# Kernel optimization log

Hardware: AMD Instinct MI355X
Metric: run time of the kernel (lower is better)

## Reference

```python
import jax, jax.numpy as jnp
import numpy as np

C = 64; H = 80; W = 160; B = 3; L = 4
REC = [4, 3, 2]  # agents per scene, sum = 9
EPS = 1e-5
NEG = -1e30  # stands in for -inf (numerically identical after softmax)


def setup_inputs() -> dict:
    key = jax.random.key(0)
    ks = jax.random.split(key, 24)
    def p(i, shape, s=0.05):
        return s * jax.random.normal(ks[i], shape, jnp.float32)
    x = jax.random.normal(ks[0], (sum(REC), C, H, W), jnp.float32)
    mask = jnp.ones((B, L, H, W), jnp.float32)
    record_len = jnp.array(REC, jnp.int32)
    eye = jnp.broadcast_to(jnp.array([[1., 0., 0.], [0., 1., 0.]], jnp.float32), (B, L, L, 2, 3))
    noise = 0.05 * jax.random.normal(ks[1], (B, L, L, 2, 3), jnp.float32)
    diag = jnp.eye(L, dtype=bool)[None, :, :, None, None]
    pairwise_t_matrix = jnp.where(diag, eye, eye + noise)  # near-identity normalized affines
    inp = dict(x=x, mask=mask, record_len=record_len, pairwise_t_matrix=pairwise_t_matrix)
    chans = [(2 * C, 128), (128, 32), (32, 8)]
    for n, (ci, co) in zip([1, 2, 3], chans):
        inp[f'w{n}'] = p(2 * n, (ci, co))
        inp[f'cb{n}'] = p(2 * n + 1, (co,), 0.01)
        inp[f'g{n}'] = 1.0 + p(8 + n, (co,), 0.1)
        inp[f'be{n}'] = p(12 + n, (co,), 0.1)
        inp[f'rm{n}'] = jnp.zeros((co,), jnp.float32)
        inp[f'rv{n}'] = jnp.ones((co,), jnp.float32)
    inp['w4'] = p(16, (8, 1)); inp['cb4'] = p(17, (1,), 0.01)
    inp['mlp_w'] = p(18, (C, C)); inp['mlp_b'] = p(19, (C,), 0.01)
    return inp


def _bilinear(feat, px, py):
    # feat [C,H,W]; px,py [H,W] source pixel coords; zero padding outside
    x0 = jnp.floor(px); y0 = jnp.floor(py)
    wx = px - x0; wy = py - y0
    x0i = x0.astype(jnp.int32); y0i = y0.astype(jnp.int32)
    def gat(xi, yi):
        inb = ((xi >= 0) & (xi < W) & (yi >= 0) & (yi < H)).astype(feat.dtype)
        v = feat[:, jnp.clip(yi, 0, H - 1), jnp.clip(xi, 0, W - 1)]
        return v * inb
    return (gat(x0i, y0i) * (1 - wx) * (1 - wy) + gat(x0i + 1, y0i) * wx * (1 - wy)
            + gat(x0i, y0i + 1) * (1 - wx) * wy + gat(x0i + 1, y0i + 1) * wx * wy)


def _warp_one(feat, theta):
    # torch affine_grid convention: src_norm = theta @ [x_n, y_n, 1]
    ys = jnp.linspace(-1.0, 1.0, H); xs = jnp.linspace(-1.0, 1.0, W)
    gx, gy = jnp.meshgrid(xs, ys)  # [H,W]
    sx = theta[0, 0] * gx + theta[0, 1] * gy + theta[0, 2]
    sy = theta[1, 0] * gx + theta[1, 1] * gy + theta[1, 2]
    px = (sx + 1.0) * (W - 1) / 2.0
    py = (sy + 1.0) * (H - 1) / 2.0
    return _bilinear(feat, px, py)

_warp_j = jax.vmap(_warp_one, in_axes=(0, 0))        # over neighbor j
_warp_ij = jax.vmap(_warp_j, in_axes=(None, 0))      # over ego i
_warp_bij = jax.vmap(_warp_ij, in_axes=(0, 0))       # over scene b


def _forward(x, mask, rec, ptm, w1, cb1, g1, be1, rm1, rv1, w2, cb2, g2, be2, rm2, rv2,
             w3, cb3, g3, be3, rm3, rv3, w4, cb4, mlp_w, mlp_b):
    # regroup: pad per-scene agent features to [B,L,C,H,W]
    feats, idx = [], 0
    for n in rec:
        feats.append(jnp.pad(x[idx:idx + n], ((0, L - n), (0, 0), (0, 0), (0, 0))))
        idx += n
    node = jnp.stack(feats)                                      # [B,L,C,H,W]
    valid = jnp.asarray((np.asarray(rec)[:, None] > np.arange(L)).astype(np.float32))  # [B,L]
    theta = jnp.swapaxes(ptm, 1, 2)                              # theta[b,i,j] = ptm[b,j,i]
    nbr = _warp_bij(node, theta)                                 # [B,L,L,C,H,W]
    wm = _warp_bij(mask[:, :, None], theta)                      # [B,L,L,1,H,W] warped ROI masks
    com_mask = wm * valid[:, None, :, None, None, None]
    ego = jnp.broadcast_to(node[:, :, None], nbr.shape)          # ego feature repeated over j
    z = jnp.concatenate([nbr, ego], axis=3)                      # [B,L,L,2C,H,W]

    def conv_bn_relu(t, w, cb, g, be, rm, rv):
        t = jnp.einsum('bijchw,co->bijohw', t, w) + cb[:, None, None]
        t = (t - rm[:, None, None]) * (g[:, None, None] / jnp.sqrt(rv[:, None, None] + EPS)) + be[:, None, None]
        return jax.nn.relu(t)

    h = conv_bn_relu(z, w1, cb1, g1, be1, rm1, rv1)
    h = conv_bn_relu(h, w2, cb2, g2, be2, rm2, rv2)
    h = conv_bn_relu(h, w3, cb3, g3, be3, rm3, rv3)
    s = jax.nn.relu(jnp.einsum('bijchw,co->bijohw', h, w4) + cb4[:, None, None])  # [B,L,L,1,H,W]
    s = jnp.where(com_mask == 0, NEG, s)
    aw = jax.nn.softmax(s, axis=2)                               # softmax over neighbors j
    updated = jnp.sum(aw * nbr * com_mask, axis=2)               # [B,L,C,H,W]
    out = updated[:, 0]                                          # ego agent per scene [B,C,H,W]
    return jnp.einsum('bchw,cd->bdhw', out, mlp_w) + mlp_b[:, None, None]


def reference(x, mask, record_len, pairwise_t_matrix, w1, cb1, g1, be1, rm1, rv1,
              w2, cb2, g2, be2, rm2, rv2, w3, cb3, g3, be3, rm3, rv3, w4, cb4, mlp_w, mlp_b):
    rec = [int(v) for v in np.asarray(record_len)]
    return _forward(x, mask, rec, pairwise_t_matrix, w1, cb1, g1, be1, rm1, rv1,
                    w2, cb2, g2, be2, rm2, rv2, w3, cb3, g3, be3, rm3, rv3, w4, cb4, mlp_w, mlp_b)
```

## Files before the change

### kernel.cpp

```cpp
#include <hip/hip_runtime.h>
#include <math.h>

#define CC 64
#define HH 80
#define WW 160
#define BB 3
#define LL 4
#define HW (HH * WW)
#define EPSf 1e-5f
#define NEGf -1e30f

typedef __attribute__((ext_vector_type(8))) short bf16x8;
typedef __attribute__((ext_vector_type(4))) float f32x4;

union BU { unsigned short s[8]; bf16x8 v; };

__device__ __forceinline__ unsigned short f2bf(float f) {
    unsigned int u = __float_as_uint(f);
    u = u + 0x7fffu + ((u >> 16) & 1u);
    return (unsigned short)(u >> 16);
}
__device__ __forceinline__ float b2f(unsigned short h) {
    return __uint_as_float(((unsigned int)h) << 16);
}

__device__ __forceinline__ void src_xy(const float* __restrict__ th, int pix,
                                       float& px, float& py) {
    int w = pix % WW, h = pix / WW;
    float gx = -1.f + 2.f * (float)w / (float)(WW - 1);
    float gy = -1.f + 2.f * (float)h / (float)(HH - 1);
    float sx = th[0] * gx + th[1] * gy + th[2];
    float sy = th[3] * gx + th[4] * gy + th[5];
    px = (sx + 1.f) * (float)(WW - 1) * 0.5f;
    py = (sy + 1.f) * (float)(HH - 1) * 0.5f;
}

struct Tap { int a00, a01, a10, a11; float w00, w01, w10, w11; };

__device__ __forceinline__ Tap mk_tap(float px, float py) {
    Tap tp;
    float x0f = floorf(px), y0f = floorf(py);
    float wx = px - x0f, wy = py - y0f;
    int x0 = (int)x0f, y0 = (int)y0f, x1 = x0 + 1, y1 = y0 + 1;
    float bx0 = (x0 >= 0 && x0 < WW) ? 1.f : 0.f;
    float bx1 = (x1 >= 0 && x1 < WW) ? 1.f : 0.f;
    float by0 = (y0 >= 0 && y0 < HH) ? 1.f : 0.f;
    float by1 = (y1 >= 0 && y1 < HH) ? 1.f : 0.f;
    int xc0 = min(max(x0, 0), WW - 1), xc1 = min(max(x1, 0), WW - 1);
    int yc0 = min(max(y0, 0), HH - 1), yc1 = min(max(y1, 0), HH - 1);
    tp.w00 = (1.f - wx) * (1.f - wy) * bx0 * by0;
    tp.w01 = wx * (1.f - wy) * bx1 * by0;
    tp.w10 = (1.f - wx) * wy * bx0 * by1;
    tp.w11 = wx * wy * bx1 * by1;
    tp.a00 = yc0 * WW + xc0; tp.a01 = yc0 * WW + xc1;
    tp.a10 = yc1 * WW + xc0; tp.a11 = yc1 * WW + xc1;
    return tp;
}


__global__ __launch_bounds__(256) void k_prep(
    const float* __restrict__ w1, const float* __restrict__ w2,
    const float* __restrict__ mlpw,
    const float* __restrict__ cb1, const float* __restrict__ g1,
    const float* __restrict__ be1, const float* __restrict__ rm1, const float* __restrict__ rv1,
    const float* __restrict__ cb2, const float* __restrict__ g2,
    const float* __restrict__ be2, const float* __restrict__ rm2, const float* __restrict__ rv2,
    const float* __restrict__ cb3, const float* __restrict__ g3,
    const float* __restrict__ be3, const float* __restrict__ rm3, const float* __restrict__ rv3,
    unsigned short* __restrict__ w1T, unsigned short* __restrict__ w2T,
    unsigned short* __restrict__ mwT,
    float* __restrict__ kk1, float* __restrict__ bb1,
    float* __restrict__ kk2, float* __restrict__ bb2,
    float* __restrict__ kk3, float* __restrict__ bb3)
{
    int idx = blockIdx.x * 256 + threadIdx.x;
    if (idx < 16384) {
        int o = idx >> 7, c = idx & 127;
        w1T[idx] = f2bf(w1[c * 128 + o]);
    } else if (idx < 20480) {
        int i = idx - 16384;
        int o2 = i >> 7, o = i & 127;
        w2T[i] = f2bf(w2[o * 32 + o2]);
    } else if (idx < 24576) {
        int i = idx - 20480;
        int d = i >> 6, c = i & 63;
        mwT[i] = f2bf(mlpw[c * 64 + d]);
    } else if (idx < 24704) {
        int o = idx - 24576;
        float k = g1[o] * rsqrtf(rv1[o] + EPSf);
        kk1[o] = k; bb1[o] = fmaf(cb1[o] - rm1[o], k, be1[o]);
    } else if (idx < 24736) {
        int o = idx - 24704;
        float k = g2[o] * rsqrtf(rv2[o] + EPSf);
        kk2[o] = k; bb2[o] = fmaf(cb2[o] - rm2[o], k, be2[o]);
    } else if (idx < 24744) {
        int o = idx - 24736;
        float k = g3[o] * rsqrtf(rv3[o] + EPSf);
        kk3[o] = k; bb3[o] = fmaf(cb3[o] - rm3[o], k, be3[o]);
    }
}


__global__ __launch_bounds__(256, 2) void k_fused(
    const float* __restrict__ x, const float* __restrict__ mask,
    const int* __restrict__ rec, const float* __restrict__ ptm,
    const unsigned short* __restrict__ w1T, const unsigned short* __restrict__ w2T,
    const unsigned short* __restrict__ mwT,
    const float* __restrict__ kk1, const float* __restrict__ bb1,
    const float* __restrict__ kk2, const float* __restrict__ bb2,
    const float* __restrict__ kk3, const float* __restrict__ bb3,
    const float* __restrict__ w3, const float* __restrict__ w4,
    const float* __restrict__ cb4, const float* __restrict__ mlp_b,
    float* __restrict__ out)
{
    __shared__ unsigned short H1s[64 * 136];
    __shared__ float H2f[64 * 36];
    __shared__ float s_s[4 * 64];
    __shared__ float com_s[4 * 64];

    int t = threadIdx.x;
    int b = blockIdx.x / 200, tile = blockIdx.x % 200;
    int pix0 = tile * 64;
    int wave = t >> 6, lane = t & 63, q = lane >> 4, r16 = lane & 15;
    int p = wave * 16 + r16;
    int pix = pix0 + p;

    int r0 = rec[0], r1 = rec[1], r2 = rec[2];
    int rb = (b == 0) ? r0 : ((b == 1) ? r1 : r2);
    int off = (b >= 1 ? r0 : 0) + (b >= 2 ? r1 : 0);

    float kv1[8], bv1[8];
    #pragma unroll
    for (int nt = 0; nt < 8; ++nt) { int o = nt * 16 + r16; kv1[nt] = kk1[o]; bv1[nt] = bb1[o]; }
    float kv2[2], bv2[2];
    #pragma unroll
    for (int nt = 0; nt < 2; ++nt) { int o = nt * 16 + r16; kv2[nt] = kk2[o]; bv2[nt] = bb2[o]; }

    bf16x8 e0, e1;
    {
        BU u0, u1;
        const float* xe = x + (size_t)off * CC * HW + pix;
        #pragma unroll
        for (int i = 0; i < 8; ++i) {
            u0.s[i] = f2bf(xe[(size_t)(q * 8 + i) * HW]);
            u1.s[i] = f2bf(xe[(size_t)(32 + q * 8 + i) * HW]);
        }
        e0 = u0.v; e1 = u1.v;
    }

    const f32x4 z4 = {0.f, 0.f, 0.f, 0.f};
    bf16x8 nbrA[8];

    #pragma unroll
    for (int j = 0; j < 4; ++j) {
        bf16x8 a0 = {0,0,0,0,0,0,0,0}, a1 = {0,0,0,0,0,0,0,0};
        bool valid = j < rb;
        if (valid) {
            const float* th = ptm + ((size_t)(b * 4 + j) * 4) * 6;
            float px, py; src_xy(th, pix, px, py);
            Tap tp = mk_tap(px, py);
            const float* feat = x + (size_t)(off + j) * CC * HW;
            BU u0, u1;
            #pragma unroll
            for (int i = 0; i < 8; ++i) {
                const float* f0 = feat + (size_t)(q * 8 + i) * HW;
                float v0 = tp.w00 * f0[tp.a00] + tp.w01 * f0[tp.a01]
                         + tp.w10 * f0[tp.a10] + tp.w11 * f0[tp.a11];
                u0.s[i] = f2bf(v0);
                const float* f1 = feat + (size_t)(32 + q * 8 + i) * HW;
                float v1 = tp.w00 * f1[tp.a00] + tp.w01 * f1[tp.a01]
                         + tp.w10 * f1[tp.a10] + tp.w11 * f1[tp.a11];
                u1.s[i] = f2bf(v1);
            }
            a0 = u0.v; a1 = u1.v;

            f32x4 acc1[8];
            #pragma unroll
            for (int nt = 0; nt < 8; ++nt) acc1[nt] = z4;
            #pragma unroll
            for (int ks = 0; ks < 4; ++ks) {
                bf16x8 A = (ks == 0) ? a0 : (ks == 1) ? a1 : (ks == 2) ? e0 : e1;
                int kcol = ks * 32 + q * 8;
                #pragma unroll
                for (int nt = 0; nt < 8; ++nt) {
                    bf16x8 bf = *(const bf16x8*)(w1T + (size_t)(nt * 16 + r16) * 128 + kcol);
                    acc1[nt] = __builtin_amdgcn_mfma_f32_16x16x32_bf16(A, bf, acc1[nt], 0, 0, 0);
                }
            }
            #pragma unroll
            for (int nt = 0; nt < 8; ++nt) {
                #pragma unroll
                for (int r = 0; r < 4; ++r) {
                    float h = fmaxf(fmaf(acc1[nt][r], kv1[nt], bv1[nt]), 0.f);
                    H1s[(wave * 16 + q * 4 + r) * 136 + nt * 16 + r16] = f2bf(h);
                }
            }
            f32x4 acc2[2]; acc2[0] = z4; acc2[1] = z4;
            #pragma unroll
            for (int ks = 0; ks < 4; ++ks) {
                int kcol = ks * 32 + q * 8;
                bf16x8 A = *(const bf16x8*)&H1s[(wave * 16 + r16) * 136 + kcol];
                #pragma unroll
                for (int nt = 0; nt < 2; ++nt) {
                    bf16x8 bf = *(const bf16x8*)(w2T + (size_t)(nt * 16 + r16) * 128 + kcol);
                    acc2[nt] = __builtin_amdgcn_mfma_f32_16x16x32_bf16(A, bf, acc2[nt], 0, 0, 0);
                }
            }
            #pragma unroll
            for (int nt = 0; nt < 2; ++nt) {
                #pragma unroll
                for (int r = 0; r < 4; ++r) {
                    float h = fmaxf(fmaf(acc2[nt][r], kv2[nt], bv2[nt]), 0.f);
                    H2f[(wave * 16 + q * 4 + r) * 36 + nt * 16 + r16] = h;
                }
            }
        }
        __syncthreads();
        if (t < 64) {
            if (valid) {
                const float* th = ptm + ((size_t)(b * 4 + j) * 4) * 6;
                float px, py; src_xy(th, pix0 + t, px, py);
                Tap tp = mk_tap(px, py);
                const float* mk = mask + (size_t)(b * 4 + j) * HW;
                float wm = tp.w00 * mk[tp.a00] + tp.w01 * mk[tp.a01]
                         + tp.w10 * mk[tp.a10] + tp.w11 * mk[tp.a11];
                float a3[8];
                #pragma unroll
                for (int o = 0; o < 8; ++o) a3[o] = 0.f;
                #pragma unroll 4
                for (int c = 0; c < 32; ++c) {
                    float hv = H2f[t * 36 + c];
                    #pragma unroll
                    for (int o = 0; o < 8; ++o) a3[o] = fmaf(hv, w3[c * 8 + o], a3[o]);
                }
                float s = cb4[0];
                #pragma unroll
                for (int o = 0; o < 8; ++o) {
                    float h = fmaxf(fmaf(a3[o], kk3[o], bb3[o]), 0.f);
                    s = fmaf(h, w4[o], s);
                }
                s = fmaxf(s, 0.f);
                s_s[j * 64 + t] = (wm == 0.f) ? NEGf : s;
                com_s[j * 64 + t] = wm;
            } else {
                s_s[j * 64 + t] = NEGf;
                com_s[j * 64 + t] = 0.f;
            }
        }
        __syncthreads();
        nbrA[j * 2 + 0] = a0;
        nbrA[j * 2 + 1] = a1;
    }

    float sj[4], cj[4];
    #pragma unroll
    for (int j = 0; j < 4; ++j) { sj[j] = s_s[j * 64 + p]; cj[j] = com_s[j * 64 + p]; }
    float m = fmaxf(fmaxf(sj[0], sj[1]), fmaxf(sj[2], sj[3]));
    float e[4], sum = 0.f;
    #pragma unroll
    for (int j = 0; j < 4; ++j) { e[j] = __expf(sj[j] - m); sum += e[j]; }
    float inv = 1.f / sum;
    float wgt[4];
    #pragma unroll
    for (int j = 0; j < 4; ++j) wgt[j] = e[j] * inv * cj[j];

    float u0f[8], u1f[8];
    #pragma unroll
    for (int i = 0; i < 8; ++i) { u0f[i] = 0.f; u1f[i] = 0.f; }
    #pragma unroll
    for (int j = 0; j < 4; ++j) {
        float wj = wgt[j];
        #pragma unroll
        for (int i = 0; i < 8; ++i) {
            u0f[i] = fmaf(wj, b2f((unsigned short)nbrA[j * 2 + 0][i]), u0f[i]);
            u1f[i] = fmaf(wj, b2f((unsigned short)nbrA[j * 2 + 1][i]), u1f[i]);
        }
    }
    BU p0, p1;
    #pragma unroll
    for (int i = 0; i < 8; ++i) { p0.s[i] = f2bf(u0f[i]); p1.s[i] = f2bf(u1f[i]); }

    f32x4 acc3[4];
    #pragma unroll
    for (int nt = 0; nt < 4; ++nt) acc3[nt] = z4;
    #pragma unroll
    for (int ks = 0; ks < 2; ++ks) {
        bf16x8 A = ks ? p1.v : p0.v;
        int kcol = ks * 32 + q * 8;
        #pragma unroll
        for (int nt = 0; nt < 4; ++nt) {
            bf16x8 bf = *(const bf16x8*)(mwT + (size_t)(nt * 16 + r16) * 64 + kcol);
            acc3[nt] = __builtin_amdgcn_mfma_f32_16x16x32_bf16(A, bf, acc3[nt], 0, 0, 0);
        }
    }

    float* outT = (float*)H1s;
    #pragma unroll
    for (int nt = 0; nt < 4; ++nt) {
        int d = nt * 16 + r16;
        float mb = mlp_b[d];
        #pragma unroll
        for (int r = 0; r < 4; ++r)
            outT[d * 65 + wave * 16 + q * 4 + r] = acc3[nt][r] + mb;
    }
    __syncthreads();
    {
        int p2 = t & 63, dg = t >> 6;
        #pragma unroll
        for (int i = 0; i < 16; ++i) {
            int d = dg * 16 + i;
            out[((size_t)(b * CC + d)) * HW + pix0 + p2] = outT[d * 65 + p2];
        }
    }
}


extern "C" void kernel_launch(void* const* d_in, const int* in_sizes, int n_in,
                              void* d_out, int out_size, void* d_ws, size_t ws_size,
                              hipStream_t stream)
{
    const float* x    = (const float*)d_in[0];
    const float* mask = (const float*)d_in[1];
    const int*   rec  = (const int*)  d_in[2];
    const float* ptm  = (const float*)d_in[3];
    const float* w1   = (const float*)d_in[4];
    const float* cb1  = (const float*)d_in[5];
    const float* g1   = (const float*)d_in[6];
    const float* be1  = (const float*)d_in[7];
    const float* rm1  = (const float*)d_in[8];
    const float* rv1  = (const float*)d_in[9];
    const float* w2   = (const float*)d_in[10];
    const float* cb2  = (const float*)d_in[11];
    const float* g2   = (const float*)d_in[12];
    const float* be2  = (const float*)d_in[13];
    const float* rm2  = (const float*)d_in[14];
    const float* rv2  = (const float*)d_in[15];
    const float* w3   = (const float*)d_in[16];
    const float* cb3  = (const float*)d_in[17];
    const float* g3   = (const float*)d_in[18];
    const float* be3  = (const float*)d_in[19];
    const float* rm3  = (const float*)d_in[20];
    const float* rv3  = (const float*)d_in[21];
    const float* w4   = (const float*)d_in[22];
    const float* cb4  = (const float*)d_in[23];
    const float* mlpw = (const float*)d_in[24];
    const float* mlpb = (const float*)d_in[25];
    float* out = (float*)d_out;

    unsigned short* w1T = (unsigned short*)d_ws;
    unsigned short* w2T = w1T + 16384;
    unsigned short* mwT = w2T + 4096;
    float* kk1 = (float*)(mwT + 4096);
    float* bb1 = kk1 + 128;
    float* kk2 = bb1 + 128;
    float* bb2 = kk2 + 32;
    float* kk3 = bb2 + 32;
    float* bb3 = kk3 + 8;

    k_prep<<<dim3(97), dim3(256), 0, stream>>>(
        w1, w2, mlpw, cb1, g1, be1, rm1, rv1, cb2, g2, be2, rm2, rv2,
        cb3, g3, be3, rm3, rv3, w1T, w2T, mwT, kk1, bb1, kk2, bb2, kk3, bb3);

    k_fused<<<dim3(600), dim3(256), 0, stream>>>(
        x, mask, rec, ptm, w1T, w2T, mwT,
        kk1, bb1, kk2, bb2, kk3, bb3,
        w3, w4, cb4, mlpb, out);
}
```

Before: 177.1 us.

## Map neighbor agents to waves with 16-pixel tiles instead of looping per block

Each block now covers 16 pixels instead of 64, and each of its four waves handles one neighbor agent in parallel. This replaces the serial loop over neighbors and its two barriers per iteration with a single barrier. Warped neighbor features go through shared memory rather than registers, and the mask-weighted score head runs in each wave's first quarter-wave. The grid grows fourfold, launch bounds target higher occupancy, and output stores become float4. The cost is that waves for absent agents sit idle, the ego features are reloaded by every wave, and the small tiles give shorter coalesced runs on gathers and stores.

Result: slower. 181.7 us (+2.6%).

```diff
diff --git a/kernel.cpp b/kernel.cpp
--- a/kernel.cpp
+++ b/kernel.cpp
@@ -101,7 +101,7 @@
 }
 
 
-__global__ __launch_bounds__(256, 2) void k_fused(
+__global__ __launch_bounds__(256, 5) void k_fused(
     const float* __restrict__ x, const float* __restrict__ mask,
     const int* __restrict__ rec, const float* __restrict__ ptm,
     const unsigned short* __restrict__ w1T, const unsigned short* __restrict__ w2T,
@@ -113,148 +113,138 @@
     const float* __restrict__ cb4, const float* __restrict__ mlp_b,
     float* __restrict__ out)
 {
-    __shared__ unsigned short H1s[64 * 136];
-    __shared__ float H2f[64 * 36];
-    __shared__ float s_s[4 * 64];
-    __shared__ float com_s[4 * 64];
+    __shared__ __align__(16) char pool[27136];
+    unsigned short* nbr_s = (unsigned short*)pool;
+    unsigned short* H1s   = (unsigned short*)(pool + 9216);
+    float* s_s   = (float*)(pool + 26624);
+    float* com_s = (float*)(pool + 26880);
 
     int t = threadIdx.x;
-    int b = blockIdx.x / 200, tile = blockIdx.x % 200;
-    int pix0 = tile * 64;
+    int b = blockIdx.x / 800, tile = blockIdx.x % 800;
+    int pix0 = tile * 16;
     int wave = t >> 6, lane = t & 63, q = lane >> 4, r16 = lane & 15;
-    int p = wave * 16 + r16;
-    int pix = pix0 + p;
+    int pix = pix0 + r16;
 
     int r0 = rec[0], r1 = rec[1], r2 = rec[2];
     int rb = (b == 0) ? r0 : ((b == 1) ? r1 : r2);
     int off = (b >= 1 ? r0 : 0) + (b >= 2 ? r1 : 0);
-
-    float kv1[8], bv1[8];
-    #pragma unroll
-    for (int nt = 0; nt < 8; ++nt) { int o = nt * 16 + r16; kv1[nt] = kk1[o]; bv1[nt] = bb1[o]; }
-    float kv2[2], bv2[2];
-    #pragma unroll
-    for (int nt = 0; nt < 2; ++nt) { int o = nt * 16 + r16; kv2[nt] = kk2[o]; bv2[nt] = bb2[o]; }
-
-    bf16x8 e0, e1;
-    {
+    bool valid = (wave < rb);
+
+    unsigned short* Hw = H1s + wave * (16 * 136);
+    float* H2w = (float*)Hw;
+    const f32x4 z4 = {0.f, 0.f, 0.f, 0.f};
+
+    if (valid) {
+        const float* th = ptm + (size_t)(b * 4 + wave) * 24;
+        float px_, py_; src_xy(th, pix, px_, py_);
+        Tap tp = mk_tap(px_, py_);
+        const float* feat = x + (size_t)(off + wave) * CC * HW;
         BU u0, u1;
+        #pragma unroll
+        for (int i = 0; i < 8; ++i) {
+            const float* f0 = feat + (size_t)(q * 8 + i) * HW;
+            float v0 = tp.w00 * f0[tp.a00] + tp.w01 * f0[tp.a01]
+                     + tp.w10 * f0[tp.a10] + tp.w11 * f0[tp.a11];
+            u0.s[i] = f2bf(v0);
+            const float* f1 = feat + (size_t)(32 + q * 8 + i) * HW;
+            float v1 = tp.w00 * f1[tp.a00] + tp.w01 * f1[tp.a01]
+                     + tp.w10 * f1[tp.a10] + tp.w11 * f1[tp.a11];
+            u1.s[i] = f2bf(v1);
+        }
+        float wm = 0.f;
+        if (q == 0) {
+            const float* mk = mask + (size_t)(b * 4 + wave) * HW;
+            wm = tp.w00 * mk[tp.a00] + tp.w01 * mk[tp.a01]
+               + tp.w10 * mk[tp.a10] + tp.w11 * mk[tp.a11];
+        }
+        *(bf16x8*)&nbr_s[(wave * 16 + r16) * 72 + q * 8]      = u0.v;
+        *(bf16x8*)&nbr_s[(wave * 16 + r16) * 72 + 32 + q * 8] = u1.v;
+
+        BU v0u, v1u;
         const float* xe = x + (size_t)off * CC * HW + pix;
         #pragma unroll
         for (int i = 0; i < 8; ++i) {
-            u0.s[i] = f2bf(xe[(size_t)(q * 8 + i) * HW]);
-            u1.s[i] = f2bf(xe[(size_t)(32 + q * 8 + i) * HW]);
-        }
-        e0 = u0.v; e1 = u1.v;
-    }
-
-    const f32x4 z4 = {0.f, 0.f, 0.f, 0.f};
-    bf16x8 nbrA[8];
-
-    #pragma unroll
-    for (int j = 0; j < 4; ++j) {
-        bf16x8 a0 = {0,0,0,0,0,0,0,0}, a1 = {0,0,0,0,0,0,0,0};
-        bool valid = j < rb;
-        if (valid) {
-            const float* th = ptm + ((size_t)(b * 4 + j) * 4) * 6;
-            float px, py; src_xy(th, pix, px, py);
-            Tap tp = mk_tap(px, py);
-            const float* feat = x + (size_t)(off + j) * CC * HW;
-            BU u0, u1;
-            #pragma unroll
-            for (int i = 0; i < 8; ++i) {
-                const float* f0 = feat + (size_t)(q * 8 + i) * HW;
-                float v0 = tp.w00 * f0[tp.a00] + tp.w01 * f0[tp.a01]
-                         + tp.w10 * f0[tp.a10] + tp.w11 * f0[tp.a11];
-                u0.s[i] = f2bf(v0);
-                const float* f1 = feat + (size_t)(32 + q * 8 + i) * HW;
-                float v1 = tp.w00 * f1[tp.a00] + tp.w01 * f1[tp.a01]
-                         + tp.w10 * f1[tp.a10] + tp.w11 * f1[tp.a11];
-                u1.s[i] = f2bf(v1);
-            }
-            a0 = u0.v; a1 = u1.v;
-
-            f32x4 acc1[8];
-            #pragma unroll
-            for (int nt = 0; nt < 8; ++nt) acc1[nt] = z4;
-            #pragma unroll
-            for (int ks = 0; ks < 4; ++ks) {
-                bf16x8 A = (ks == 0) ? a0 : (ks == 1) ? a1 : (ks == 2) ? e0 : e1;
-                int kcol = ks * 32 + q * 8;
+            v0u.s[i] = f2bf(xe[(size_t)(q * 8 + i) * HW]);
+            v1u.s[i] = f2bf(xe[(size_t)(32 + q * 8 + i) * HW]);
+        }
+
+        f32x4 acc1[8];
+        #pragma unroll
+        for (int nt = 0; nt < 8; ++nt) acc1[nt] = z4;
+        #pragma unroll
+        for (int ks = 0; ks < 4; ++ks) {
+            bf16x8 A = (ks == 0) ? u0.v : (ks == 1) ? u1.v : (ks == 2) ? v0u.v : v1u.v;
+            int kcol = ks * 32 + q * 8;
+            #pragma unroll
+            for (int nt = 0; nt < 8; ++nt) {
+                bf16x8 bw = *(const bf16x8*)(w1T + (size_t)(nt * 16 + r16) * 128 + kcol);
+                acc1[nt] = __builtin_amdgcn_mfma_f32_16x16x32_bf16(A, bw, acc1[nt], 0, 0, 0);
+            }
+        }
+        #pragma unroll
+        for (int nt = 0; nt < 8; ++nt) {
+            int o = nt * 16 + r16;
+            float kv = kk1[o], bv = bb1[o];
+            #pragma unroll
+            for (int r = 0; r < 4; ++r) {
+                float h = fmaxf(fmaf(acc1[nt][r], kv, bv), 0.f);
+                Hw[(q * 4 + r) * 136 + o] = f2bf(h);
+            }
+        }
+
+        f32x4 acc2[2]; acc2[0] = z4; acc2[1] = z4;
+        #pragma unroll
+        for (int ks = 0; ks < 4; ++ks) {
+            int kcol = ks * 32 + q * 8;
+            bf16x8 A = *(const bf16x8*)&Hw[r16 * 136 + kcol];
+            #pragma unroll
+            for (int nt = 0; nt < 2; ++nt) {
+                bf16x8 bw = *(const bf16x8*)(w2T + (size_t)(nt * 16 + r16) * 128 + kcol);
+                acc2[nt] = __builtin_amdgcn_mfma_f32_16x16x32_bf16(A, bw, acc2[nt], 0, 0, 0);
+            }
+        }
+        #pragma unroll
+        for (int nt = 0; nt < 2; ++nt) {
+            int o = nt * 16 + r16;
+            float kv = kk2[o], bv = bb2[o];
+            #pragma unroll
+            for (int r = 0; r < 4; ++r) {
+                float h = fmaxf(fmaf(acc2[nt][r], kv, bv), 0.f);
+                H2w[(q * 4 + r) * 36 + o] = h;
+            }
+        }
+
+        if (q == 0) {
+            float a3[8];
+            #pragma unroll
+            for (int o = 0; o < 8; ++o) a3[o] = 0.f;
+            #pragma unroll 4
+            for (int c = 0; c < 32; ++c) {
+                float hv = H2w[r16 * 36 + c];
                 #pragma unroll
-                for (int nt = 0; nt < 8; ++nt) {
-                    bf16x8 bf = *(const bf16x8*)(w1T + (size_t)(nt * 16 + r16) * 128 + kcol);
-                    acc1[nt] = __builtin_amdgcn_mfma_f32_16x16x32_bf16(A, bf, acc1[nt], 0, 0, 0);
-                }
-            }
-            #pragma unroll
-            for (int nt = 0; nt < 8; ++nt) {
-                #pragma unroll
-                for (int r = 0; r < 4; ++r) {
-                    float h = fmaxf(fmaf(acc1[nt][r], kv1[nt], bv1[nt]), 0.f);
-                    H1s[(wave * 16 + q * 4 + r) * 136 + nt * 16 + r16] = f2bf(h);
-                }
-            }
-            f32x4 acc2[2]; acc2[0] = z4; acc2[1] = z4;
-            #pragma unroll
-            for (int ks = 0; ks < 4; ++ks) {
-                int kcol = ks * 32 + q * 8;
-                bf16x8 A = *(const bf16x8*)&H1s[(wave * 16 + r16) * 136 + kcol];
-                #pragma unroll
-                for (int nt = 0; nt < 2; ++nt) {
-                    bf16x8 bf = *(const bf16x8*)(w2T + (size_t)(nt * 16 + r16) * 128 + kcol);
-                    acc2[nt] = __builtin_amdgcn_mfma_f32_16x16x32_bf16(A, bf, acc2[nt], 0, 0, 0);
-                }
-            }
-            #pragma unroll
-            for (int nt = 0; nt < 2; ++nt) {
-                #pragma unroll
-                for (int r = 0; r < 4; ++r) {
-                    float h = fmaxf(fmaf(acc2[nt][r], kv2[nt], bv2[nt]), 0.f);
-                    H2f[(wave * 16 + q * 4 + r) * 36 + nt * 16 + r16] = h;
-                }
-            }
-        }
-        __syncthreads();
-        if (t < 64) {
-            if (valid) {
-                const float* th = ptm + ((size_t)(b * 4 + j) * 4) * 6;
-                float px, py; src_xy(th, pix0 + t, px, py);
-                Tap tp = mk_tap(px, py);
-                const float* mk = mask + (size_t)(b * 4 + j) * HW;
-                float wm = tp.w00 * mk[tp.a00] + tp.w01 * mk[tp.a01]
-                         + tp.w10 * mk[tp.a10] + tp.w11 * mk[tp.a11];
-                float a3[8];
-                #pragma unroll
-                for (int o = 0; o < 8; ++o) a3[o] = 0.f;
-                #pragma unroll 4
-                for (int c = 0; c < 32; ++c) {
-                    float hv = H2f[t * 36 + c];
-                    #pragma unroll
-                    for (int o = 0; o < 8; ++o) a3[o] = fmaf(hv, w3[c * 8 + o], a3[o]);
-                }
-                float s = cb4[0];
-                #pragma unroll
-                for (int o = 0; o < 8; ++o) {
-                    float h = fmaxf(fmaf(a3[o], kk3[o], bb3[o]), 0.f);
-                    s = fmaf(h, w4[o], s);
-                }
-                s = fmaxf(s, 0.f);
-                s_s[j * 64 + t] = (wm == 0.f) ? NEGf : s;
-                com_s[j * 64 + t] = wm;
-            } else {
-                s_s[j * 64 + t] = NEGf;
-                com_s[j * 64 + t] = 0.f;
-            }
-        }
-        __syncthreads();
-        nbrA[j * 2 + 0] = a0;
-        nbrA[j * 2 + 1] = a1;
-    }
+                for (int o = 0; o < 8; ++o) a3[o] = fmaf(hv, w3[c * 8 + o], a3[o]);
+            }
+            float s = cb4[0];
+            #pragma unroll
+            for (int o = 0; o < 8; ++o) {
+                float h = fmaxf(fmaf(a3[o], kk3[o], bb3[o]), 0.f);
+                s = fmaf(h, w4[o], s);
+            }
+            s = fmaxf(s, 0.f);
+            s_s[wave * 16 + r16]   = (wm == 0.f) ? NEGf : s;
+            com_s[wave * 16 + r16] = wm;
+        }
+    } else {
+        bf16x8 zb = {0, 0, 0, 0, 0, 0, 0, 0};
+        *(bf16x8*)&nbr_s[(wave * 16 + r16) * 72 + q * 8]      = zb;
+        *(bf16x8*)&nbr_s[(wave * 16 + r16) * 72 + 32 + q * 8] = zb;
+        if (q == 0) { s_s[wave * 16 + r16] = NEGf; com_s[wave * 16 + r16] = 0.f; }
+    }
+    __syncthreads();
 
     float sj[4], cj[4];
     #pragma unroll
-    for (int j = 0; j < 4; ++j) { sj[j] = s_s[j * 64 + p]; cj[j] = com_s[j * 64 + p]; }
+    for (int j = 0; j < 4; ++j) { sj[j] = s_s[j * 16 + r16]; cj[j] = com_s[j * 16 + r16]; }
     float m = fmaxf(fmaxf(sj[0], sj[1]), fmaxf(sj[2], sj[3]));
     float e[4], sum = 0.f;
     #pragma unroll
@@ -264,53 +254,46 @@
     #pragma unroll
     for (int j = 0; j < 4; ++j) wgt[j] = e[j] * inv * cj[j];
 
-    float u0f[8], u1f[8];
-    #pragma unroll
-    for (int i = 0; i < 8; ++i) { u0f[i] = 0.f; u1f[i] = 0.f; }
+    float uf0[8], uf1[8];
+    #pragma unroll
+    for (int i = 0; i < 8; ++i) { uf0[i] = 0.f; uf1[i] = 0.f; }
     #pragma unroll
     for (int j = 0; j < 4; ++j) {
         float wj = wgt[j];
+        bf16x8 n0 = *(const bf16x8*)&nbr_s[(j * 16 + r16) * 72 + q * 8];
+        bf16x8 n1 = *(const bf16x8*)&nbr_s[(j * 16 + r16) * 72 + 32 + q * 8];
         #pragma unroll
         for (int i = 0; i < 8; ++i) {
-            u0f[i] = fmaf(wj, b2f((unsigned short)nbrA[j * 2 + 0][i]), u0f[i]);
-            u1f[i] = fmaf(wj, b2f((unsigned short)nbrA[j * 2 + 1][i]), u1f[i]);
+            uf0[i] = fmaf(wj, b2f((unsigned short)n0[i]), uf0[i]);
+            uf1[i] = fmaf(wj, b2f((unsigned short)n1[i]), uf1[i]);
         }
     }
     BU p0, p1;
     #pragma unroll
-    for (int i = 0; i < 8; ++i) { p0.s[i] = f2bf(u0f[i]); p1.s[i] = f2bf(u1f[i]); }
-
-    f32x4 acc3[4];
-    #pragma unroll
-    for (int nt = 0; nt < 4; ++nt) acc3[nt] = z4;
+    for (int i = 0; i < 8; ++i) { p0.s[i] = f2bf(uf0[i]); p1.s[i] = f2bf(uf1[i]); }
+
+    f32x4 acc3 = z4;
     #pragma unroll
     for (int ks = 0; ks < 2; ++ks) {
         bf16x8 A = ks ? p1.v : p0.v;
-        int kcol = ks * 32 + q * 8;
-        #pragma unroll
-        for (int nt = 0; nt < 4; ++nt) {
-            bf16x8 bf = *(const bf16x8*)(mwT + (size_t)(nt * 16 + r16) * 64 + kcol);
-            acc3[nt] = __builtin_amdgcn_mfma_f32_16x16x32_bf16(A, bf, acc3[nt], 0, 0, 0);
-        }
-    }
-
-    float* outT = (float*)H1s;
-    #pragma unroll
-    for (int nt = 0; nt < 4; ++nt) {
-        int d = nt * 16 + r16;
+        bf16x8 bw = *(const bf16x8*)(mwT + (size_t)(wave * 16 + r16) * 64 + ks * 32 + q * 8);
+        acc3 = __builtin_amdgcn_mfma_f32_16x16x32_bf16(A, bw, acc3, 0, 0, 0);
+    }
+    __syncthreads();
+
+    float* outT = (float*)pool;
+    {
+        int d = wave * 16 + r16;
         float mb = mlp_b[d];
         #pragma unroll
         for (int r = 0; r < 4; ++r)
-            outT[d * 65 + wave * 16 + q * 4 + r] = acc3[nt][r] + mb;
+            outT[d * 20 + q * 4 + r] = acc3[r] + mb;
     }
     __syncthreads();
     {
-        int p2 = t & 63, dg = t >> 6;
-        #pragma unroll
-        for (int i = 0; i < 16; ++i) {
-            int d = dg * 16 + i;
-            out[((size_t)(b * CC + d)) * HW + pix0 + p2] = outT[d * 65 + p2];
-        }
+        int d = t >> 2, c4 = (t & 3) * 4;
+        float4 v = *(const float4*)&outT[d * 20 + c4];
+        *(float4*)&out[((size_t)(b * CC + d)) * HW + pix0 + c4] = v;
     }
 }
 
@@ -361,7 +344,7 @@
         w1, w2, mlpw, cb1, g1, be1, rm1, rv1, cb2, g2, be2, rm2, rv2,
         cb3, g3, be3, rm3, rv3, w1T, w2T, mwT, kk1, bb1, kk2, bb2, kk3, bb3);
 
-    k_fused<<<dim3(600), dim3(256), 0, stream>>>(
+    k_fused<<<dim3(2400), dim3(256), 0, stream>>>(
         x, mask, rec, ptm, w1T, w2T, mwT,
         kk1, bb1, kk2, bb2, kk3, bb3,
         w3, w4, cb4, mlpb, out);
```
